# Kernel tuning notes

Measured on AMD Instinct MI355X. Metric: run time of the kernel, lower is better.

## Reference

```python
import jax, jax.numpy as jnp
import numpy as np

SQ23 = float(np.sqrt(2.0 / 3.0))
WIDTH = 1.0  # Fem.width

NELEM = 500_000
NGP = 4
NNODE = 250_000
NDOF = NNODE * 2
HID = 64


def setup_inputs() -> dict:
    key = jax.random.key(0)
    ks = jax.random.split(key, 12)
    u = jax.random.normal(ks[0], (NDOF,), jnp.float32)
    B = jax.random.normal(ks[1], (NELEM, NGP, 3, 8), jnp.float32)
    Jacc = jax.random.uniform(ks[2], (NELEM, NGP), jnp.float32, 0.1, 1.0)
    gp_w = jnp.ones((NGP,), jnp.float32)
    connectivity = jax.random.randint(ks[3], (NELEM, 4), 0, NNODE, jnp.int32)
    weight1 = jax.random.normal(ks[4], (NDOF,), jnp.float32) / 10.0
    scales_inp = jnp.ones((2,), jnp.float32)
    limits_inp = jnp.zeros((2,), jnp.float32)
    scales_grad = jnp.ones((2,), jnp.float32)
    limits_grad = jnp.zeros((2,), jnp.float32)
    W1 = jax.random.normal(ks[5], (2, HID), jnp.float32) / np.sqrt(2.0)
    b1 = jnp.zeros((HID,), jnp.float32)
    W2 = jax.random.normal(ks[6], (HID, HID), jnp.float32) / np.sqrt(HID)
    b2 = jnp.zeros((HID,), jnp.float32)
    W3 = jax.random.normal(ks[7], (HID, 2), jnp.float32) / np.sqrt(HID)
    b3 = jnp.zeros((2,), jnp.float32)
    return dict(u=u, B=B, Jacc=Jacc, gp_w=gp_w, connectivity=connectivity,
                weight1=weight1, scales_inp=scales_inp, limits_inp=limits_inp,
                scales_grad=scales_grad, limits_grad=limits_grad,
                W1=W1, b1=b1, W2=W2, b2=b2, W3=W3, b3=b3)


def reference(u, B, Jacc, gp_w, connectivity, weight1, scales_inp, limits_inp,
              scales_grad, limits_grad, W1, b1, W2, b2, W3, b3):
    ndof = u.shape[0]
    # u_torch1: masked scaling of displacements (all DOFs free here)
    u1 = weight1 * u
    # elemental DOF indices: [E, 8] interleaved (2n, 2n+1) per node
    conn = connectivity
    edofs = jnp.stack([2 * conn, 2 * conn + 1], axis=-1).reshape(conn.shape[0], -1)
    u_e = u1[edofs]                                  # [E, 8] gather
    strain = jnp.einsum('egij,ej->egi', B, u_e)      # [E, G, 3] Voigt strain
    s0, s1, s2 = strain[..., 0], strain[..., 1], strain[..., 2]
    # strain invariants: volumetric ev, deviatoric es, direction n
    ev = s0 + s1
    d00 = s0 - ev / 3.0
    d11 = s1 - ev / 3.0
    d22 = -ev / 3.0
    d01 = s2 / 2.0
    det = jnp.sqrt(d00**2 + d11**2 + d22**2 + 2.0 * d01**2)
    n00, n11, n01 = d00 / det, d11 / det, d01 / det
    es = det * SQ23
    # normalize inputs to the sub-model
    ns = jnp.stack([ev * scales_inp[0] + limits_inp[0],
                    es * scales_inp[1] + limits_inp[1]], axis=-1)  # [E, G, 2]
    # sub-model MLP (batched over all elements x gauss points)
    h = jnp.tanh(ns @ W1 + b1)
    h = jnp.tanh(h @ W2 + b2)
    g = h @ W3 + b3                                  # [E, G, 2]
    # un-normalize -> (p, q) invariants
    p = (g[..., 0] - limits_grad[0]) / scales_grad[0]
    q = (g[..., 1] - limits_grad[1]) / scales_grad[1]
    # invariants -> Voigt stress [s00, s11, s01]
    c = SQ23 * q
    sv = jnp.stack([p + c * n00, p + c * n11, c * n01], axis=-1)  # [E, G, 3]
    # per-GP weights and elemental force: sum_g B^T sigma * (width*Jacc*w_g)
    w = WIDTH * Jacc * gp_w[None, :]                 # [E, G]
    E_P = jnp.einsum('egij,egi,eg->ej', B, sv, w)    # [E, 8]
    # scatter-add assemblage into global force vector
    F = jnp.zeros(ndof, u.dtype).at[edofs.reshape(-1)].add(E_P.reshape(-1))
    return F
```

## Files before the change

kernel.cpp:

```cpp
#include <hip/hip_runtime.h>

#define NELEM 500000
#define NDOF 500000
#define NNODE 250000
#define HID 64
#define NT 31250
#define NBLK 1024
#define NWAVE (NBLK * 4)

typedef _Float16 half2v __attribute__((ext_vector_type(2)));
typedef _Float16 half8v __attribute__((ext_vector_type(8)));
typedef float float4v __attribute__((ext_vector_type(4)));

#define LAM 2.885390081777927f
#define FSCALE 4194304.0f
#define FINV   2.384185791015625e-7f

__device__ __forceinline__ half2v pk(float a, float b) {
    return __builtin_bit_cast(half2v, __builtin_amdgcn_cvt_pkrtz(a, b));
}
__device__ __forceinline__ float tanh2(float y) {
    float e = __builtin_amdgcn_exp2f(y);
    float r = __builtin_amdgcn_rcpf(e + 1.0f);
    return fmaf(-2.0f, r, 1.0f);
}
__device__ __forceinline__ float fdot2(half2v a, half2v b, float c) {
    return __builtin_amdgcn_fdot2(a, b, c, false);
}

#define SWZF(x, pat) __builtin_bit_cast(float, \
    __builtin_amdgcn_ds_swizzle(__builtin_bit_cast(int, (x)), (pat)))

__global__ __launch_bounds__(64, 1) void pack_weights(
    const float* __restrict__ W2, uint4* __restrict__ ws)
{
    const int lane = threadIdx.x & 63;
    const int quad = lane >> 4, l15 = lane & 15;
#pragma unroll
    for (int t = 0; t < 4; t++)
#pragma unroll
        for (int f = 0; f < 2; f++) {
            union { uint4 q; uint u[4]; } T;
#pragma unroll
            for (int jj = 0; jj < 4; jj++) {
                const int k0 = f * 32 + quad * 8 + 2 * jj;
                const int n  = t * 16 + l15;
                T.u[jj] = __builtin_bit_cast(uint,
                    pk(LAM * W2[k0 * HID + n], LAM * W2[(k0 + 1) * HID + n]));
            }
            ws[(8 + 2 * t + f) * 64 + lane] = T.q;
        }
}

__global__ __launch_bounds__(256, 8) void premul_u(
    const float* __restrict__ u, const float* __restrict__ w1,
    float* __restrict__ u1)
{
    const int i = blockIdx.x * 256 + threadIdx.x;
    if (i < NDOF / 4) {
        const float4 a = ((const float4*)u)[i];
        const float4 b = ((const float4*)w1)[i];
        ((float4*)u1)[i] = make_float4(a.x * b.x, a.y * b.y, a.z * b.z, a.w * b.w);
    }
}

__global__ __launch_bounds__(256, 8) void convert_F(unsigned long long* __restrict__ F64)
{
    const int i = blockIdx.x * 256 + threadIdx.x;
    if (i < NNODE) {
        const unsigned long long v = F64[i];
        const int lo = (int)(unsigned)(v & 0xFFFFFFFFull);
        const int hi = (int)(unsigned)(v >> 32);
        float2 out = make_float2((float)lo * FINV, (float)hi * FINV);
        *(float2*)&F64[i] = out;
    }
}

#define TSTEP(tt, qa, qb) do { \
    const float4v b2v = *(const float4v*)&b2t[wb + (tt) * 4]; \
    union { uint4 q; uint u[4]; } w3u; \
    w3u.q = *(const uint4*)&w3t[wb + (tt) * 4]; \
    float4v c = b2v; \
    c = __builtin_amdgcn_mfma_f32_16x16x32_f16(__builtin_bit_cast(half8v, (qa)), B0.v, c, 0, 0, 0); \
    c = __builtin_amdgcn_mfma_f32_16x16x32_f16(__builtin_bit_cast(half8v, (qb)), B1.v, c, 0, 0, 0); \
    _Pragma("unroll") \
    for (int reg = 0; reg < 4; reg++) { \
        const float h = tanh2(c[reg]); \
        const half2v hh = pk(h, h); \
        sp = sp + hh * __builtin_bit_cast(half2v, w3u.u[reg]); \
    } \
} while (0)

__global__ __launch_bounds__(256, 4) void fem_force_kernel(
    const float* __restrict__ u, const float* __restrict__ B,
    const float* __restrict__ Jacc, const float* __restrict__ gp_w,
    const int* __restrict__ conn, const float* __restrict__ weight1,
    const float* __restrict__ scales_inp, const float* __restrict__ limits_inp,
    const float* __restrict__ scales_grad, const float* __restrict__ limits_grad,
    const float* __restrict__ W1, const float* __restrict__ b1,
    const float* __restrict__ b2, const float* __restrict__ W3,
    const float* __restrict__ b3, const uint4* __restrict__ wt,
    const int premul, unsigned long long* __restrict__ F64)
{
    __shared__ uint sPQ[8 * 260];
    __shared__ uint sXs[4][64];
    __shared__ uint sGs[4][64];
    __shared__ __align__(16) float b2t[64];
    __shared__ __align__(16) uint  w3t[64];
    __shared__ __align__(16) uint  w1tb[4][16];
    __shared__ __align__(16) float b1tb[4][16];

    const int tid  = threadIdx.x;
    const int lane = tid & 63;
    const int wv   = tid >> 6;
    const int quad = lane >> 4;
    const int l15  = lane & 15;
    const int g    = lane & 3;
    const int pqb  = wv * 65;

    if (tid < 64) {
        const int i  = tid;
        const int it = (i >> 2) & 3, iq = i >> 4, ir = i & 3;
        const int n  = it * 16 + iq * 4 + ir;
        b2t[i] = LAM * b2[n];
        w3t[i] = __builtin_bit_cast(uint, pk(W3[2 * n], W3[2 * n + 1]));
    } else if (tid < 128) {
        const int i = tid - 64;
        const int q = i >> 4, idx = i & 15, f = idx >> 3, jj = idx & 7;
        const int k = f * 32 + q * 8 + jj;
        w1tb[q][idx] = __builtin_bit_cast(uint, pk(LAM * W1[k], LAM * W1[HID + k]));
    } else if (tid < 192) {
        const int i = tid - 128;
        const int q = i >> 4, idx = i & 15, f = idx >> 3, jj = idx & 7;
        const int k = f * 32 + q * 8 + jj;
        b1tb[q][idx] = LAM * b1[k];
    }
    __syncthreads();

    const float SQ23 = 0.816496580927726f;
    const float si0 = scales_inp[0], si1 = scales_inp[1];
    const float li0 = limits_inp[0], li1 = limits_inp[1];
    const float isg0 = 1.0f / scales_grad[0], isg1 = 1.0f / scales_grad[1];
    const float b30c = b3[0] - limits_grad[0];
    const float b31c = b3[1] - limits_grad[1];
    const float gw  = gp_w[g];

    uint4 bfq[8];
#pragma unroll
    for (int i = 0; i < 8; i++) bfq[i] = wt[(8 + i) * 64 + lane];
#pragma unroll
    for (int i = 0; i < 8; i++)
        asm volatile("" : "+v"(bfq[i].x), "+v"(bfq[i].y), "+v"(bfq[i].z), "+v"(bfq[i].w));

    int T = blockIdx.x * 4 + wv;
    float4 bq0, bq1, bq2, bq3, bq4, bq5;
    {
        const float4* Bp = (const float4*)(B + (size_t)T * 1536 + lane * 24);
        bq0 = Bp[0]; bq1 = Bp[1]; bq2 = Bp[2];
        bq3 = Bp[3]; bq4 = Bp[4]; bq5 = Bp[5];
    }
    int connT = conn[T * 64 + lane];
    float jacT = Jacc[T * 64 + lane];
    float2 uT = *(const float2*)(u + 2 * connT);
    float2 wvT = make_float2(1.f, 1.f);
    if (!premul) wvT = *(const float2*)(weight1 + 2 * connT);

    int connN = 0;
    float2 uN = make_float2(0.f, 0.f), wvN = make_float2(1.f, 1.f);
    float jacN = 0.f;

#pragma unroll 1
    for (; T < NT; T += NWAVE) {
        const int Tn = T + NWAVE;
        const bool hasN = (Tn < NT);
        if (hasN) {
            connN = conn[Tn * 64 + lane];
            jacN  = Jacc[Tn * 64 + lane];
        }

        {
            const float vx = wvT.x * uT.x, vy = wvT.y * uT.y;
            float ue[8];
            ue[0] = SWZF(vx, 0x1C); ue[1] = SWZF(vy, 0x1C);
            ue[2] = SWZF(vx, 0x3C); ue[3] = SWZF(vy, 0x3C);
            ue[4] = SWZF(vx, 0x5C); ue[5] = SWZF(vy, 0x5C);
            ue[6] = SWZF(vx, 0x7C); ue[7] = SWZF(vy, 0x7C);

            float Bg[24];
            Bg[0]=bq0.x; Bg[1]=bq0.y; Bg[2]=bq0.z; Bg[3]=bq0.w;
            Bg[4]=bq1.x; Bg[5]=bq1.y; Bg[6]=bq1.z; Bg[7]=bq1.w;
            Bg[8]=bq2.x; Bg[9]=bq2.y; Bg[10]=bq2.z; Bg[11]=bq2.w;
            Bg[12]=bq3.x; Bg[13]=bq3.y; Bg[14]=bq3.z; Bg[15]=bq3.w;
            Bg[16]=bq4.x; Bg[17]=bq4.y; Bg[18]=bq4.z; Bg[19]=bq4.w;
            Bg[20]=bq5.x; Bg[21]=bq5.y; Bg[22]=bq5.z; Bg[23]=bq5.w;

            float s0 = 0.f, s1 = 0.f, s2 = 0.f;
#pragma unroll
            for (int j = 0; j < 8; j++) {
                s0 = fmaf(Bg[j],      ue[j], s0);
                s1 = fmaf(Bg[8 + j],  ue[j], s1);
                s2 = fmaf(Bg[16 + j], ue[j], s2);
            }
            const float ev  = s0 + s1;
            const float ev3 = ev * (1.0f / 3.0f);
            const float d00 = s0 - ev3, d11 = s1 - ev3, d22 = -ev3, d01 = 0.5f * s2;
            const float det = sqrtf(d00 * d00 + d11 * d11 + d22 * d22 + 2.0f * d01 * d01);
            const float rd  = __builtin_amdgcn_rcpf(det);
            const float es  = det * SQ23;
            const float wgt = jacT * gw;
            const float sc  = SQ23 * rd * wgt;
            const float c00 = sc * d00, c11 = sc * d11, c01 = sc * d01;
#pragma unroll
            for (int j = 0; j < 8; j++) {
                const float P = wgt * (Bg[j] + Bg[8 + j]);
                const float Q = fmaf(c00, Bg[j], fmaf(c11, Bg[8 + j], c01 * Bg[16 + j]));
                sPQ[j * 260 + pqb + lane] = __builtin_bit_cast(uint, pk(P, Q));
            }
            sXs[wv][lane] = __builtin_bit_cast(uint,
                pk(fmaf(ev, si0, li0), fmaf(es, si1, li1)));
        }
        if (hasN) {
            const float4* Bp = (const float4*)(B + (size_t)Tn * 1536 + lane * 24);
            bq0 = Bp[0]; bq1 = Bp[1]; bq2 = Bp[2];
            bq3 = Bp[3]; bq4 = Bp[4]; bq5 = Bp[5];
        }
        asm volatile("s_waitcnt lgkmcnt(0)");
        __builtin_amdgcn_sched_barrier(0);
        if (hasN) {
            uN = *(const float2*)(u + 2 * connN);
            if (!premul) wvN = *(const float2*)(weight1 + 2 * connN);
        }

        int zr = 0;
#pragma unroll 1
        for (int rt = 0; rt < 4; rt++) {
            asm volatile("" : "+v"(zr));
            const int qz = quad + zr;
            const int wb = qz * 16;
            const half2v xp = __builtin_bit_cast(half2v, sXs[wv][rt * 16 + l15]);

            union { uint4 q[4]; uint u[16]; } W1L;
            union { float4 q[4]; float f[16]; } B1L;
#pragma unroll
            for (int i = 0; i < 4; i++) {
                W1L.q[i] = *(const uint4*)&w1tb[qz][4 * i];
                B1L.q[i] = *(const float4*)&b1tb[qz][4 * i];
            }

            union { half8v v; uint uu[4]; } B0, B1;
#pragma unroll
            for (int jj = 0; jj < 4; jj++) {
                const float t0 = tanh2(fdot2(xp, __builtin_bit_cast(half2v, W1L.u[2 * jj]),     B1L.f[2 * jj]));
                const float t1 = tanh2(fdot2(xp, __builtin_bit_cast(half2v, W1L.u[2 * jj + 1]), B1L.f[2 * jj + 1]));
                const float t2 = tanh2(fdot2(xp, __builtin_bit_cast(half2v, W1L.u[8 + 2 * jj]),     B1L.f[8 + 2 * jj]));
                const float t3 = tanh2(fdot2(xp, __builtin_bit_cast(half2v, W1L.u[8 + 2 * jj + 1]), B1L.f[8 + 2 * jj + 1]));
                B0.uu[jj] = __builtin_bit_cast(uint, pk(t0, t1));
                B1.uu[jj] = __builtin_bit_cast(uint, pk(t2, t3));
            }

            half2v sp = {_Float16(0.f), _Float16(0.f)};
            TSTEP(0, bfq[0], bfq[1]);
            TSTEP(1, bfq[2], bfq[3]);
            TSTEP(2, bfq[4], bfq[5]);
            TSTEP(3, bfq[6], bfq[7]);

            float s0 = (float)sp[0], s1 = (float)sp[1];
            s0 += SWZF(s0, 0x401F);
            s1 += SWZF(s1, 0x401F);
            s0 += __shfl_xor(s0, 32, 64);
            s1 += __shfl_xor(s1, 32, 64);
            if (quad == 0) {
                const float p = (s0 + b30c) * isg0;
                const float q = (s1 + b31c) * isg1;
                sGs[wv][rt * 16 + l15] = __builtin_bit_cast(uint, pk(p, q));
            }
        }
        asm volatile("s_waitcnt vmcnt(0) lgkmcnt(0)");
        __builtin_amdgcn_sched_barrier(0);

        {
            const int rb = lane & ~3;
            const int j0 = 2 * g;
            float a = 0.f, b = 0.f;
#pragma unroll
            for (int gp = 0; gp < 4; gp++) {
                const int rr = rb + gp;
                const half2v pq = __builtin_bit_cast(half2v, sGs[wv][rr]);
                const uint w0 = sPQ[j0 * 260 + pqb + rr];
                const uint w1 = sPQ[(j0 + 1) * 260 + pqb + rr];
                a = fdot2(pq, __builtin_bit_cast(half2v, w0), a);
                b = fdot2(pq, __builtin_bit_cast(half2v, w1), b);
            }
            const int ia = __float2int_rn(a * FSCALE);
            const int ib = __float2int_rn(b * FSCALE);
            const unsigned long long pkd =
                ((unsigned long long)(unsigned)ib << 32) | (unsigned)ia;
            atomicAdd(&F64[connT], pkd);
        }

        connT = connN; uT = uN; jacT = jacN; wvT = wvN;
    }
}

extern "C" void kernel_launch(void* const* d_in, const int* in_sizes, int n_in,
                              void* d_out, int out_size, void* d_ws, size_t ws_size,
                              hipStream_t stream) {
    const float* u           = (const float*)d_in[0];
    const float* B           = (const float*)d_in[1];
    const float* Jacc        = (const float*)d_in[2];
    const float* gp_w        = (const float*)d_in[3];
    const int*   conn        = (const int*)  d_in[4];
    const float* weight1     = (const float*)d_in[5];
    const float* scales_inp  = (const float*)d_in[6];
    const float* limits_inp  = (const float*)d_in[7];
    const float* scales_grad = (const float*)d_in[8];
    const float* limits_grad = (const float*)d_in[9];
    const float* W1          = (const float*)d_in[10];
    const float* b1          = (const float*)d_in[11];
    const float* W2          = (const float*)d_in[12];
    const float* b2          = (const float*)d_in[13];
    const float* W3          = (const float*)d_in[14];
    const float* b3          = (const float*)d_in[15];
    unsigned long long* F64 = (unsigned long long*)d_out;

    uint4* wt = (uint4*)d_ws;
    float* u1 = (float*)((char*)d_ws + 16384);
    const int can_premul = (ws_size >= 16384 + sizeof(float) * NDOF) ? 1 : 0;

    (void)hipMemsetAsync(d_out, 0, sizeof(float) * NDOF, stream);

    pack_weights<<<1, 64, 0, stream>>>(W2, wt);
    if (can_premul)
        premul_u<<<(NDOF / 4 + 255) / 256, 256, 0, stream>>>(u, weight1, u1);

    fem_force_kernel<<<NBLK, 256, 0, stream>>>(
        can_premul ? u1 : u, B, Jacc, gp_w, conn, weight1,
        scales_inp, limits_inp, scales_grad, limits_grad,
        W1, b1, b2, W3, b3, wt, can_premul, F64);

    convert_F<<<(NNODE + 255) / 256, 256, 0, stream>>>(F64);
}
```

Before: 354.6 us.

## Privatize force accumulation per XCC with workgroup-scope atomics

Each block reads its XCC ID from a hardware register and does its 64-bit packed fixed-point atomic adds into one of eight private copies of the force vector, kept in workspace. The adds use relaxed workgroup-scope atomics, so they can resolve in that XCC's L2 instead of needing device-wide coherence. The conversion kernel then sums the eight copies before converting back to float. In exchange the code zeroes a 16 MB buffer and reads it back in the reduction. It also depends on the atomics staying correct when several workgroups on the same XCC hit the same addresses under workgroup scope.

Result: slower. 363.0 us (+2.4%).

```diff
diff --git a/kernel.cpp b/kernel.cpp
--- a/kernel.cpp
+++ b/kernel.cpp
@@ -7,6 +7,7 @@
 #define NT 31250
 #define NBLK 1024
 #define NWAVE (NBLK * 4)
+#define CSTRIDE 262144
 
 typedef _Float16 half2v __attribute__((ext_vector_type(2)));
 typedef _Float16 half8v __attribute__((ext_vector_type(8)));
@@ -64,15 +65,23 @@
     }
 }
 
-__global__ __launch_bounds__(256, 8) void convert_F(unsigned long long* __restrict__ F64)
+__global__ __launch_bounds__(256, 8) void convert_F(
+    unsigned long long* __restrict__ F64,
+    const unsigned long long* __restrict__ F8, const int priv)
 {
     const int i = blockIdx.x * 256 + threadIdx.x;
     if (i < NNODE) {
-        const unsigned long long v = F64[i];
+        unsigned long long v;
+        if (priv) {
+            v = 0ull;
+#pragma unroll
+            for (int x = 0; x < 8; x++) v += F8[(size_t)x * CSTRIDE + i];
+        } else {
+            v = F64[i];
+        }
         const int lo = (int)(unsigned)(v & 0xFFFFFFFFull);
         const int hi = (int)(unsigned)(v >> 32);
-        float2 out = make_float2((float)lo * FINV, (float)hi * FINV);
-        *(float2*)&F64[i] = out;
+        *(float2*)&F64[i] = make_float2((float)lo * FINV, (float)hi * FINV);
     }
 }
 
@@ -100,7 +109,9 @@
     const float* __restrict__ W1, const float* __restrict__ b1,
     const float* __restrict__ b2, const float* __restrict__ W3,
     const float* __restrict__ b3, const uint4* __restrict__ wt,
-    const int premul, unsigned long long* __restrict__ F64)
+    const int premul, const int priv,
+    unsigned long long* __restrict__ F64,
+    unsigned long long* __restrict__ F8)
 {
     __shared__ uint sPQ[8 * 260];
     __shared__ uint sXs[4][64];
@@ -117,6 +128,10 @@
     const int l15  = lane & 15;
     const int g    = lane & 3;
     const int pqb  = wv * 65;
+
+    uint xcc;
+    asm volatile("s_getreg_b32 %0, hwreg(HW_REG_XCC_ID)" : "=s"(xcc));
+    unsigned long long* Fp = F8 + (size_t)(xcc & 7) * CSTRIDE;
 
     if (tid < 64) {
         const int i  = tid;
@@ -295,7 +310,13 @@
             const int ib = __float2int_rn(b * FSCALE);
             const unsigned long long pkd =
                 ((unsigned long long)(unsigned)ib << 32) | (unsigned)ia;
-            atomicAdd(&F64[connT], pkd);
+            if (priv) {
+                __hip_atomic_fetch_add(Fp + connT, pkd,
+                                       __ATOMIC_RELAXED,
+                                       __HIP_MEMORY_SCOPE_WORKGROUP);
+            } else {
+                atomicAdd(&F64[connT], pkd);
+            }
         }
 
         connT = connN; uT = uN; jacT = jacN; wvT = wvN;
@@ -325,9 +346,16 @@
 
     uint4* wt = (uint4*)d_ws;
     float* u1 = (float*)((char*)d_ws + 16384);
+    unsigned long long* F8 =
+        (unsigned long long*)((char*)d_ws + 16384 + 2097152);
+    const size_t priv_bytes = (size_t)8 * CSTRIDE * 8;
     const int can_premul = (ws_size >= 16384 + sizeof(float) * NDOF) ? 1 : 0;
+    const int can_priv   =
+        (ws_size >= 16384 + 2097152 + priv_bytes) ? 1 : 0;
 
     (void)hipMemsetAsync(d_out, 0, sizeof(float) * NDOF, stream);
+    if (can_priv)
+        (void)hipMemsetAsync(F8, 0, priv_bytes, stream);
 
     pack_weights<<<1, 64, 0, stream>>>(W2, wt);
     if (can_premul)
@@ -336,7 +364,7 @@
     fem_force_kernel<<<NBLK, 256, 0, stream>>>(
         can_premul ? u1 : u, B, Jacc, gp_w, conn, weight1,
         scales_inp, limits_inp, scales_grad, limits_grad,
-        W1, b1, b2, W3, b3, wt, can_premul, F64);
-
-    convert_F<<<(NNODE + 255) / 256, 256, 0, stream>>>(F64);
-}
+        W1, b1, b2, W3, b3, wt, can_premul, can_priv, F64, F8);
+
+    convert_F<<<(NNODE + 255) / 256, 256, 0, stream>>>(F64, F8, can_priv);
+}
```
